# Performance work log

Measured on AMD Instinct MI355X. Metric: run time of the kernel, lower is better.

Reference implementation:

```python
import jax, jax.numpy as jnp
import numpy as np

B, N, D, H = 32, 512, 1024, 16
HD = D // H          # head_dim = 64
SEG = 64             # seg_num (router set size, softmax axis)
FACTOR = N           # einsum forces factor == seq_len


def setup_inputs() -> dict:
    key = jax.random.key(0)
    ks = jax.random.split(key, 12)
    s = 0.02
    return {
        "query": jax.random.normal(ks[0], (B, N, D), jnp.float32),
        "key":   jax.random.normal(ks[1], (B, N, D), jnp.float32),
        "value": jax.random.normal(ks[2], (B, N, D), jnp.float32),
        "router": jax.random.normal(ks[3], (SEG, FACTOR, HD), jnp.float32),
        "Wq": jax.random.normal(ks[4], (D, D), jnp.float32) * s,
        "bq": jnp.zeros((D,), jnp.float32),
        "Wk": jax.random.normal(ks[5], (D, D), jnp.float32) * s,
        "bk": jnp.zeros((D,), jnp.float32),
        "Wv": jax.random.normal(ks[6], (D, D), jnp.float32) * s,
        "bv": jnp.zeros((D,), jnp.float32),
        "Wo": jax.random.normal(ks[7], (D, D), jnp.float32) * s,
        "bo": jnp.zeros((D,), jnp.float32),
    }


def reference(query, key, value, router, Wq, bq, Wk, bk, Wv, bv, Wo, bo):
    b = query.shape[0]
    q = query @ Wq + bq                      # (B, N, D)
    k = key @ Wk + bk                        # computed but unused (faithful to source)
    v = value @ Wv + bv                      # computed but unused (faithful to source)
    # (B, N, H, HD) -> (B, H, N, HD)
    qh = q.reshape(b, -1, H, HD).transpose(0, 2, 1, 3)
    # torch: einsum('bnhd,bfhd->bnhf', q_bHnd, router_bSFd); shared 'h' = seq/factor
    # scores: (B, H, N, SEG); softmax over router/segment axis
    scores = jnp.einsum('bhnd,snd->bhns', qh, router)
    attn = jax.nn.softmax(scores, axis=-1)   # dropout = identity (eval mode)
    # combine: (B, H, N, HD)
    received = jnp.einsum('bhns,snd->bhnd', attn, router)
    received = received.transpose(0, 2, 1, 3).reshape(b, -1, D)
    output = received @ Wo + bo              # (B, N, D)
    return output, attn
```

## Files before the change

### kernel.cpp

```cpp
#include <hip/hip_runtime.h>

#define DEV __device__ __forceinline__

typedef __attribute__((ext_vector_type(8))) short bf16x8;
typedef __attribute__((ext_vector_type(4))) float f32x4;

constexpr int Bc  = 32;
constexpr int Nc  = 512;
constexpr int Dc  = 1024;
constexpr int Hc  = 16;
constexpr int HDc = 64;
constexpr int SEGc= 64;
constexpr int Mrows = Bc * Nc;

DEV unsigned short bf16r(float x) {
  union { float f; unsigned int u; } c; c.f = x;
  unsigned int r = (c.u + 0x7fffu + ((c.u >> 16) & 1u)) >> 16;
  return (unsigned short)r;
}

DEV void async_ld16(const void* g, void* l) {
  __builtin_amdgcn_global_load_lds(
      (const __attribute__((address_space(1))) void*)g,
      (__attribute__((address_space(3))) void*)l,
      16, 0, 0);
}

__global__ __launch_bounds__(256)
void prep(const float* __restrict__ Wq, const float* __restrict__ Wo,
          const float* __restrict__ router,
          unsigned short* __restrict__ wqt, unsigned short* __restrict__ WoT,
          unsigned short* __restrict__ Rg, unsigned short* __restrict__ RTg) {
  const int bid = blockIdx.x;
  if (bid < 2048) {
    __shared__ float tile[32][33];
    const bool isWq = bid < 1024;
    const int b2 = isWq ? bid : bid - 1024;
    const float* src = isWq ? Wq : Wo;
    const int bx = b2 & 31, by = b2 >> 5;
    const int tx = threadIdx.x & 31, ty = threadIdx.x >> 5;
    for (int i = 0; i < 4; ++i) {
      int r = ty + i * 8;
      tile[r][tx] = src[(size_t)(by * 32 + r) * 1024 + bx * 32 + tx];
    }
    __syncthreads();
    if (isWq) {
      if (ty < 4) {
        const int oct = ty;
        const int c = bx * 32 + tx, cbb = c >> 9, cl = c & 511;
        const int cphys = cl ^ (oct << 1);
        unsigned short tmp[8];
#pragma unroll
        for (int e = 0; e < 8; ++e) tmp[e] = bf16r(tile[oct * 8 + e][tx]);
        ushort4 u0, u1;
        u0.x = tmp[0]; u0.y = tmp[1]; u0.z = tmp[2]; u0.w = tmp[3];
        u1.x = tmp[4]; u1.y = tmp[5]; u1.z = tmp[6]; u1.w = tmp[7];
        size_t idx = (size_t)cbb * 524288 + (size_t)by * 16384
                   + (size_t)oct * 4096 + (size_t)cphys * 8;
        *(ushort4*)(wqt + idx)     = u0;
        *(ushort4*)(wqt + idx + 4) = u1;
      }
    } else {
      for (int i = 0; i < 4; ++i) {
        int r = ty + i * 8;
        WoT[(size_t)(bx * 32 + r) * 1024 + by * 32 + tx] = bf16r(tile[tx][r]);
      }
    }
  } else {
    const int nn = bid - 2048;
    const int t  = threadIdx.x;
    const int s  = t >> 2, dq = (t & 3) * 16;
    const float* p = router + ((size_t)s * 512 + nn) * 64 + dq;
    float v[16];
#pragma unroll
    for (int i = 0; i < 16; i += 4) {
      float4 f = *(const float4*)(p + i);
      v[i] = f.x; v[i+1] = f.y; v[i+2] = f.z; v[i+3] = f.w;
    }
    unsigned short bvv[16];
#pragma unroll
    for (int i = 0; i < 16; ++i) bvv[i] = bf16r(v[i]);
    unsigned short* rb = Rg + (size_t)nn * 4096 + s * 64;
#pragma unroll
    for (int o2 = 0; o2 < 2; ++o2) {
      int oct  = (dq >> 3) + o2;
      int phys = oct ^ (s & 7);
      ushort4 a, b2v;
      a.x   = bvv[o2*8+0]; a.y   = bvv[o2*8+1]; a.z   = bvv[o2*8+2]; a.w   = bvv[o2*8+3];
      b2v.x = bvv[o2*8+4]; b2v.y = bvv[o2*8+5]; b2v.z = bvv[o2*8+6]; b2v.w = bvv[o2*8+7];
      *(ushort4*)(rb + phys * 8)     = a;
      *(ushort4*)(rb + phys * 8 + 4) = b2v;
    }
    unsigned short* tb = RTg + (size_t)nn * 4096;
#pragma unroll
    for (int i = 0; i < 16; ++i) {
      int d = dq + i;
      tb[d * 64 + (((s >> 3) ^ (d & 7)) * 8) + (s & 7)] = bvv[i];
    }
  }
}

template <bool OUT_F32>
__global__ __launch_bounds__(256)
void gemm_bt(const unsigned short* __restrict__ A,
             const unsigned short* __restrict__ BT,
             const float* __restrict__ bias,
             void* __restrict__ Cout) {
  constexpr int K = 1024, Nn = 1024, BM = 128, BK = 32;
  __shared__ unsigned short As[BM * BK];
  __shared__ unsigned short Bs[BM * BK];
  const int tid = threadIdx.x, lane = tid & 63, wave = tid >> 6;
  const int tm = blockIdx.x >> 3, tn = blockIdx.x & 7;
  const int wm = (wave >> 1) * 64, wn = (wave & 1) * 64;
  const int la = lane & 15, quad = lane >> 4, lb8 = quad * 8;

  f32x4 acc[4][4] = {};

  const int srow = tid >> 2;
  const int scol = (tid & 3) * 8;
  const unsigned short* Ag = A  + (size_t)(tm * BM + srow) * K + scol;
  const unsigned short* Bg = BT + (size_t)(tn * BM + srow) * K + scol;
  unsigned short* ldsA = As + wave * 512;
  unsigned short* ldsB = Bs + wave * 512;

  for (int k0 = 0; k0 < K; k0 += BK) {
    __syncthreads();
    async_ld16(Ag + k0,          ldsA);
    async_ld16(Ag + 64 * K + k0, ldsA + 2048);
    async_ld16(Bg + k0,          ldsB);
    async_ld16(Bg + 64 * K + k0, ldsB + 2048);
    __syncthreads();

    bf16x8 af[4], bfr[4];
#pragma unroll
    for (int i = 0; i < 4; ++i)
      af[i] = *(const bf16x8*)(As + (wm + i * 16 + la) * BK + lb8);
#pragma unroll
    for (int j = 0; j < 4; ++j)
      bfr[j] = *(const bf16x8*)(Bs + (wn + j * 16 + la) * BK + lb8);
#pragma unroll
    for (int i = 0; i < 4; ++i)
#pragma unroll
      for (int j = 0; j < 4; ++j)
        acc[i][j] = __builtin_amdgcn_mfma_f32_16x16x32_bf16(af[i], bfr[j],
                                                            acc[i][j], 0, 0, 0);
  }

  const int colbase = tn * BM + wn;
  float bv[4];
#pragma unroll
  for (int j = 0; j < 4; ++j) bv[j] = bias[colbase + j * 16 + la];

  float* eps = (wave < 2) ? ((float*)As) + wave * 1024
                          : ((float*)Bs) + (wave - 2) * 1024;
  const int rowbase = tm * BM + wm;

#pragma unroll
  for (int i = 0; i < 4; ++i) {
    __syncthreads();
#pragma unroll
    for (int j = 0; j < 4; ++j)
#pragma unroll
      for (int r = 0; r < 4; ++r)
        eps[(quad * 4 + r) * 64 + j * 16 + la] = acc[i][j][r] + bv[j];
    __syncthreads();
#pragma unroll
    for (int s = 0; s < 4; ++s) {
      int idx = s * 64 + lane;
      int row = idx >> 4, c4 = idx & 15;
      float4 v = *(const float4*)(eps + row * 64 + c4 * 4);
      size_t goff = (size_t)(rowbase + i * 16 + row) * Nn + colbase + c4 * 4;
      if (OUT_F32) {
        *(float4*)((float*)Cout + goff) = v;
      } else {
        ushort4 u;
        u.x = bf16r(v.x); u.y = bf16r(v.y); u.z = bf16r(v.z); u.w = bf16r(v.w);
        *(ushort4*)((unsigned short*)Cout + goff) = u;
      }
    }
  }
}

__global__ __launch_bounds__(512)
void fused_qmid(const float* __restrict__ query,
                const unsigned short* __restrict__ wqt,
                const float* __restrict__ bq,
                const unsigned short* __restrict__ Rg,
                const unsigned short* __restrict__ RTg,
                float* __restrict__ attn_out,
                unsigned short* __restrict__ recv_out) {
  __shared__ __align__(16) unsigned short lds[36864];
  const int tid = threadIdx.x, lane = tid & 63, w = tid >> 6;
  const int la = lane & 15, quad = lane >> 4;
  const int n0 = (blockIdx.x >> 1) * 2, cbh = blockIdx.x & 1;

  f32x4 acc[4][4] = {};

  const int arow = tid >> 3;
  const int ag   = tid & 7;
  const int a_b  = arow & 31, a_nl = arow >> 5;
  const float* aq = query + ((size_t)(a_b * 512 + n0 + a_nl)) * 1024 + ag * 4;
  const int a_oct  = ag >> 1;
  const int a_lidx = a_oct * 512 + (arow ^ (a_oct << 1)) * 8 + (ag & 1) * 4;
  const int bslot  = w * 512 + lane * 8;
  const unsigned short* wqb = wqt + (size_t)cbh * 524288;

  {
    float4 qv = *(const float4*)(aq);
#pragma unroll
    for (int p = 0; p < 4; ++p)
      async_ld16(wqb + p * 4096 + bslot, lds + p * 4096 + w * 512);
    ushort4 u;
    u.x = bf16r(qv.x); u.y = bf16r(qv.y); u.z = bf16r(qv.z); u.w = bf16r(qv.w);
    *(ushort4*)(lds + 32768 + a_lidx) = u;
  }
  __syncthreads();

#pragma unroll 1
  for (int kb = 0; kb < 32; ++kb) {
    const int cur = kb & 1;
    unsigned short* Bc_ = lds + cur * 16384;
    unsigned short* Ac_ = lds + 32768 + cur * 2048;
    unsigned short* Bn_ = lds + (cur ^ 1) * 16384;
    unsigned short* An_ = lds + 32768 + (cur ^ 1) * 2048;

    float4 qv;
    if (kb < 31) {
      qv = *(const float4*)(aq + (kb + 1) * 32);
#pragma unroll
      for (int p = 0; p < 4; ++p)
        async_ld16(wqb + (size_t)(kb + 1) * 16384 + p * 4096 + bslot,
                   Bn_ + p * 4096 + w * 512);
    } else {
#pragma unroll
      for (int q2 = 0; q2 < 4; ++q2) {
        const unsigned short* srcb = (q2 < 2)
            ? (Rg  + (size_t)(n0 + q2)     * 4096)
            : (RTg + (size_t)(n0 + q2 - 2) * 4096);
        async_ld16(srcb + bslot, lds + q2 * 4096 + w * 512);
      }
    }

    bf16x8 af[4], bfr[4];
#pragma unroll
    for (int rt = 0; rt < 4; ++rt)
      af[rt] = *(const bf16x8*)(Ac_ + quad * 512
                                + ((rt * 16 + la) ^ (quad << 1)) * 8);
#pragma unroll
    for (int j = 0; j < 4; ++j)
      bfr[j] = *(const bf16x8*)(Bc_ + quad * 4096
                                + (((w * 4 + j) * 16 + la) ^ (quad << 1)) * 8);
#pragma unroll
    for (int rt = 0; rt < 4; ++rt)
#pragma unroll
      for (int j = 0; j < 4; ++j)
        acc[rt][j] = __builtin_amdgcn_mfma_f32_16x16x32_bf16(af[rt], bfr[j],
                                                             acc[rt][j], 0, 0, 0);
    if (kb < 31) {
      ushort4 u;
      u.x = bf16r(qv.x); u.y = bf16r(qv.y); u.z = bf16r(qv.z); u.w = bf16r(qv.w);
      *(ushort4*)(An_ + a_lidx) = u;
    }
    __syncthreads();
  }

  float bv[4];
#pragma unroll
  for (int j = 0; j < 4; ++j) bv[j] = bq[cbh * 512 + (w * 4 + j) * 16 + la];
#pragma unroll
  for (int rt = 0; rt < 4; ++rt)
#pragma unroll
    for (int j = 0; j < 4; ++j)
#pragma unroll
      for (int r = 0; r < 4; ++r) acc[rt][j][r] += bv[j];

  const int h = cbh * 8 + w;
  unsigned short* QA = lds + 16384 + w * 2304;

#pragma unroll
  for (int nl = 0; nl < 2; ++nl) {
    const int nn = n0 + nl;

#pragma unroll
    for (int rt2 = 0; rt2 < 2; ++rt2)
#pragma unroll
      for (int j4 = 0; j4 < 4; ++j4)
#pragma unroll
        for (int r = 0; r < 4; ++r)
          QA[(rt2 * 16 + quad * 4 + r) * 72 + j4 * 16 + la]
              = bf16r(acc[nl * 2 + rt2][j4][r]);

    bf16x8 qf[2][2], rf[4][2];
#pragma unroll
    for (int bt = 0; bt < 2; ++bt)
#pragma unroll
      for (int kc = 0; kc < 2; ++kc)
        qf[bt][kc] = *(const bf16x8*)(QA + (bt * 16 + la) * 72
                                      + (kc * 4 + quad) * 8);
    const unsigned short* Rn = lds + nl * 4096;
#pragma unroll
    for (int st = 0; st < 4; ++st)
#pragma unroll
      for (int kc = 0; kc < 2; ++kc) {
        int s_ = st * 16 + la;
        rf[st][kc] = *(const bf16x8*)(Rn + s_ * 64
                                      + ((kc * 4 + quad) ^ (s_ & 7)) * 8);
      }

    f32x4 sacc[2][4] = {};
#pragma unroll
    for (int bt = 0; bt < 2; ++bt)
#pragma unroll
      for (int st = 0; st < 4; ++st) {
        sacc[bt][st] = __builtin_amdgcn_mfma_f32_16x16x32_bf16(rf[st][0], qf[bt][0], sacc[bt][st], 0, 0, 0);
        sacc[bt][st] = __builtin_amdgcn_mfma_f32_16x16x32_bf16(rf[st][1], qf[bt][1], sacc[bt][st], 0, 0, 0);
      }

#pragma unroll
    for (int bt = 0; bt < 2; ++bt) {
      float mx = sacc[bt][0][0];
#pragma unroll
      for (int st = 0; st < 4; ++st)
#pragma unroll
        for (int r = 0; r < 4; ++r) mx = fmaxf(mx, sacc[bt][st][r]);
      mx = fmaxf(mx, __shfl_xor(mx, 16));
      mx = fmaxf(mx, __shfl_xor(mx, 32));
      float sum = 0.f;
#pragma unroll
      for (int st = 0; st < 4; ++st)
#pragma unroll
        for (int r = 0; r < 4; ++r) {
          float e = __expf(sacc[bt][st][r] - mx);
          sacc[bt][st][r] = e; sum += e;
        }
      sum += __shfl_xor(sum, 16);
      sum += __shfl_xor(sum, 32);
      float inv = 1.0f / sum;
#pragma unroll
      for (int st = 0; st < 4; ++st) {
        sacc[bt][st][0] *= inv; sacc[bt][st][1] *= inv;
        sacc[bt][st][2] *= inv; sacc[bt][st][3] *= inv;
      }
      const int b_ = bt * 16 + la;
      float* ao = attn_out + ((size_t)(b_ * 16 + h) * 512 + nn) * 64 + quad * 4;
#pragma unroll
      for (int st = 0; st < 4; ++st) {
        *(float4*)(ao + st * 16) = *(float4*)(&sacc[bt][st]);
        ushort4 u;
        u.x = bf16r(sacc[bt][st][0]); u.y = bf16r(sacc[bt][st][1]);
        u.z = bf16r(sacc[bt][st][2]); u.w = bf16r(sacc[bt][st][3]);
        *(ushort4*)(QA + b_ * 72 + st * 16 + quad * 4) = u;
      }
    }

    __asm__ volatile("s_waitcnt lgkmcnt(0)" ::: "memory");
    bf16x8 atf[2][2], rtf2[4][2];
#pragma unroll
    for (int bt = 0; bt < 2; ++bt)
#pragma unroll
      for (int kc = 0; kc < 2; ++kc)
        atf[bt][kc] = *(const bf16x8*)(QA + (bt * 16 + la) * 72
                                       + (kc * 4 + quad) * 8);
    const unsigned short* RTn = lds + 8192 + nl * 4096;
#pragma unroll
    for (int dt = 0; dt < 4; ++dt)
#pragma unroll
      for (int kc = 0; kc < 2; ++kc) {
        int d_ = dt * 16 + la;
        rtf2[dt][kc] = *(const bf16x8*)(RTn + d_ * 64
                                        + ((kc * 4 + quad) ^ (d_ & 7)) * 8);
      }
    f32x4 racc[2][4] = {};
#pragma unroll
    for (int bt = 0; bt < 2; ++bt)
#pragma unroll
      for (int dt = 0; dt < 4; ++dt) {
        racc[bt][dt] = __builtin_amdgcn_mfma_f32_16x16x32_bf16(rtf2[dt][0], atf[bt][0], racc[bt][dt], 0, 0, 0);
        racc[bt][dt] = __builtin_amdgcn_mfma_f32_16x16x32_bf16(rtf2[dt][1], atf[bt][1], racc[bt][dt], 0, 0, 0);
      }

#pragma unroll
    for (int bt = 0; bt < 2; ++bt) {
      const int b_ = bt * 16 + la;
      unsigned short* ro = recv_out + ((size_t)(b_ * 512 + nn)) * 1024
                         + h * 64 + quad * 4;
#pragma unroll
      for (int dt = 0; dt < 4; ++dt) {
        ushort4 u;
        u.x = bf16r(racc[bt][dt][0]); u.y = bf16r(racc[bt][dt][1]);
        u.z = bf16r(racc[bt][dt][2]); u.w = bf16r(racc[bt][dt][3]);
        *(ushort4*)(ro + dt * 16) = u;
      }
    }
  }
}

extern "C" void kernel_launch(void* const* d_in, const int* in_sizes, int n_in,
                              void* d_out, int out_size, void* d_ws, size_t ws_size,
                              hipStream_t stream) {
  const float* query  = (const float*)d_in[0];
  const float* router = (const float*)d_in[3];
  const float* Wq     = (const float*)d_in[4];
  const float* bq     = (const float*)d_in[5];
  const float* Wo     = (const float*)d_in[10];
  const float* bo     = (const float*)d_in[11];

  float* out      = (float*)d_out;
  float* attn_out = out + (size_t)Bc * Nc * Dc;

  char* ws = (char*)d_ws;
  unsigned short* recv_b = (unsigned short*)(ws);
  unsigned short* WqTile = (unsigned short*)(ws + 33554432u);
  unsigned short* WoT    = (unsigned short*)(ws + 35651584u);
  unsigned short* Rg     = (unsigned short*)(ws + 37748736u);
  unsigned short* RTg    = (unsigned short*)(ws + 41943040u);

  prep         <<<2560, 256, 0, stream>>>(Wq, Wo, router, WqTile, WoT, Rg, RTg);
  fused_qmid   <<<512,  512, 0, stream>>>(query, WqTile, bq, Rg, RTg,
                                          attn_out, recv_b);
  gemm_bt<true><<<(Mrows / 128) * 8, 256, 0, stream>>>(recv_b, WoT, bo, out);
}
```

Measured before the change: 378.9 us.

## Pre-convert query to bf16 and pipeline GEMMs with register A-fragments

The prep kernel now also converts the fp32 query to bf16, and Wo is repacked into a swizzled tiled layout. Both GEMM kernels load A fragments straight from global memory into registers and double-buffer only B in per-wave LDS. They wait with s_waitcnt vmcnt instead of block-wide barriers inside the K loop. This is meant to drop the per-iteration __syncthreads and the in-loop fp32-to-bf16 conversion, and to halve query read bandwidth in the main kernel. The cost is an extra 32 MB bf16 write plus re-read of query, and a wider occupancy hint in the launch bounds.

```diff
diff --git a/kernel.cpp b/kernel.cpp
--- a/kernel.cpp
+++ b/kernel.cpp
@@ -28,9 +28,10 @@
 
 __global__ __launch_bounds__(256)
 void prep(const float* __restrict__ Wq, const float* __restrict__ Wo,
-          const float* __restrict__ router,
-          unsigned short* __restrict__ wqt, unsigned short* __restrict__ WoT,
-          unsigned short* __restrict__ Rg, unsigned short* __restrict__ RTg) {
+          const float* __restrict__ router, const float* __restrict__ query,
+          unsigned short* __restrict__ wqt, unsigned short* __restrict__ wot,
+          unsigned short* __restrict__ Rg, unsigned short* __restrict__ RTg,
+          unsigned short* __restrict__ qb) {
   const int bid = blockIdx.x;
   if (bid < 2048) {
     __shared__ float tile[32][33];
@@ -44,29 +45,29 @@
       tile[r][tx] = src[(size_t)(by * 32 + r) * 1024 + bx * 32 + tx];
     }
     __syncthreads();
-    if (isWq) {
-      if (ty < 4) {
-        const int oct = ty;
-        const int c = bx * 32 + tx, cbb = c >> 9, cl = c & 511;
-        const int cphys = cl ^ (oct << 1);
-        unsigned short tmp[8];
-#pragma unroll
-        for (int e = 0; e < 8; ++e) tmp[e] = bf16r(tile[oct * 8 + e][tx]);
-        ushort4 u0, u1;
-        u0.x = tmp[0]; u0.y = tmp[1]; u0.z = tmp[2]; u0.w = tmp[3];
-        u1.x = tmp[4]; u1.y = tmp[5]; u1.z = tmp[6]; u1.w = tmp[7];
-        size_t idx = (size_t)cbb * 524288 + (size_t)by * 16384
-                   + (size_t)oct * 4096 + (size_t)cphys * 8;
-        *(ushort4*)(wqt + idx)     = u0;
-        *(ushort4*)(wqt + idx + 4) = u1;
-      }
-    } else {
-      for (int i = 0; i < 4; ++i) {
-        int r = ty + i * 8;
-        WoT[(size_t)(bx * 32 + r) * 1024 + by * 32 + tx] = bf16r(tile[tx][r]);
-      }
-    }
-  } else {
+    if (ty < 4) {
+      const int oct = ty;
+      const int c = bx * 32 + tx;
+      unsigned short tmp[8];
+#pragma unroll
+      for (int e = 0; e < 8; ++e) tmp[e] = bf16r(tile[oct * 8 + e][tx]);
+      ushort4 u0, u1;
+      u0.x = tmp[0]; u0.y = tmp[1]; u0.z = tmp[2]; u0.w = tmp[3];
+      u1.x = tmp[4]; u1.y = tmp[5]; u1.z = tmp[6]; u1.w = tmp[7];
+      size_t idx;
+      if (isWq) {
+        const int cbb = c >> 9, cl = c & 511;
+        idx = (size_t)cbb * 524288 + (size_t)by * 16384
+            + (size_t)oct * 4096 + (size_t)(cl ^ (oct << 1)) * 8;
+        *(ushort4*)(wqt + idx) = u0; *(ushort4*)(wqt + idx + 4) = u1;
+      } else {
+        const int tn = c >> 7, cl = c & 127;
+        idx = (size_t)tn * 131072 + (size_t)by * 4096
+            + (size_t)oct * 1024 + (size_t)(cl ^ (oct << 1)) * 8;
+        *(ushort4*)(wot + idx) = u0; *(ushort4*)(wot + idx + 4) = u1;
+      }
+    }
+  } else if (bid < 2560) {
     const int nn = bid - 2048;
     const int t  = threadIdx.x;
     const int s  = t >> 2, dq = (t & 3) * 16;
@@ -97,63 +98,91 @@
       int d = dq + i;
       tb[d * 64 + (((s >> 3) ^ (d & 7)) * 8) + (s & 7)] = bvv[i];
     }
-  }
-}
-
-template <bool OUT_F32>
-__global__ __launch_bounds__(256)
+  } else {
+    const size_t base = ((size_t)(bid - 2560) * 256 + threadIdx.x) * 8;
+    float4 a = *(const float4*)(query + base);
+    float4 b = *(const float4*)(query + base + 4);
+    ushort4 u0, u1;
+    u0.x = bf16r(a.x); u0.y = bf16r(a.y); u0.z = bf16r(a.z); u0.w = bf16r(a.w);
+    u1.x = bf16r(b.x); u1.y = bf16r(b.y); u1.z = bf16r(b.z); u1.w = bf16r(b.w);
+    *(ushort4*)(qb + base)     = u0;
+    *(ushort4*)(qb + base + 4) = u1;
+  }
+}
+
+__global__ __launch_bounds__(256, 4)
 void gemm_bt(const unsigned short* __restrict__ A,
-             const unsigned short* __restrict__ BT,
+             const unsigned short* __restrict__ wot,
              const float* __restrict__ bias,
-             void* __restrict__ Cout) {
-  constexpr int K = 1024, Nn = 1024, BM = 128, BK = 32;
-  __shared__ unsigned short As[BM * BK];
-  __shared__ unsigned short Bs[BM * BK];
+             float* __restrict__ Cout) {
+  __shared__ __align__(16) unsigned short lds[16384];
   const int tid = threadIdx.x, lane = tid & 63, wave = tid >> 6;
   const int tm = blockIdx.x >> 3, tn = blockIdx.x & 7;
   const int wm = (wave >> 1) * 64, wn = (wave & 1) * 64;
-  const int la = lane & 15, quad = lane >> 4, lb8 = quad * 8;
+  const int la = lane & 15, quad = lane >> 4;
 
   f32x4 acc[4][4] = {};
 
-  const int srow = tid >> 2;
-  const int scol = (tid & 3) * 8;
-  const unsigned short* Ag = A  + (size_t)(tm * BM + srow) * K + scol;
-  const unsigned short* Bg = BT + (size_t)(tn * BM + srow) * K + scol;
-  unsigned short* ldsA = As + wave * 512;
-  unsigned short* ldsB = Bs + wave * 512;
-
-  for (int k0 = 0; k0 < K; k0 += BK) {
-    __syncthreads();
-    async_ld16(Ag + k0,          ldsA);
-    async_ld16(Ag + 64 * K + k0, ldsA + 2048);
-    async_ld16(Bg + k0,          ldsB);
-    async_ld16(Bg + 64 * K + k0, ldsB + 2048);
-    __syncthreads();
-
-    bf16x8 af[4], bfr[4];
-#pragma unroll
-    for (int i = 0; i < 4; ++i)
-      af[i] = *(const bf16x8*)(As + (wm + i * 16 + la) * BK + lb8);
+  const unsigned short* aA[4];
+#pragma unroll
+  for (int rt = 0; rt < 4; ++rt)
+    aA[rt] = A + (size_t)(tm * 128 + wm + rt * 16 + la) * 1024 + quad * 8;
+  const unsigned short* wob = wot + (size_t)tn * 131072 + wn * 8 + lane * 8;
+  unsigned short* wlds = lds + wave * 2048;
+
+  bf16x8 afA[4], afB[4];
+  {
+#pragma unroll
+    for (int rt = 0; rt < 4; ++rt) afA[rt] = *(const bf16x8*)(aA[rt]);
+#pragma unroll
+    for (int p = 0; p < 4; ++p)
+      async_ld16(wob + p * 1024, wlds + p * 512);
+  }
+  __builtin_amdgcn_sched_barrier(0);
+
+  auto step = [&](int kb, bf16x8* afc, bf16x8* afn,
+                  unsigned short* Bc_, unsigned short* Bn_,
+                  bool last) __attribute__((always_inline)) {
+    if (!last) {
+#pragma unroll
+      for (int rt = 0; rt < 4; ++rt)
+        afn[rt] = *(const bf16x8*)(aA[rt] + (kb + 1) * 32);
+#pragma unroll
+      for (int p = 0; p < 4; ++p)
+        async_ld16(wob + (size_t)(kb + 1) * 4096 + p * 1024, Bn_ + p * 512);
+    }
+    __builtin_amdgcn_sched_barrier(0);
+    if (!last) asm volatile("s_waitcnt vmcnt(8)" ::: "memory");
+    else       asm volatile("s_waitcnt vmcnt(0)" ::: "memory");
+    __builtin_amdgcn_sched_barrier(0);
+    bf16x8 bfr[4];
 #pragma unroll
     for (int j = 0; j < 4; ++j)
-      bfr[j] = *(const bf16x8*)(Bs + (wn + j * 16 + la) * BK + lb8);
-#pragma unroll
-    for (int i = 0; i < 4; ++i)
+      bfr[j] = *(const bf16x8*)(Bc_ + quad * 512
+                                + ((j * 16 + la) ^ (quad << 1)) * 8);
+#pragma unroll
+    for (int rt = 0; rt < 4; ++rt)
 #pragma unroll
       for (int j = 0; j < 4; ++j)
-        acc[i][j] = __builtin_amdgcn_mfma_f32_16x16x32_bf16(af[i], bfr[j],
-                                                            acc[i][j], 0, 0, 0);
-  }
-
-  const int colbase = tn * BM + wn;
+        acc[rt][j] = __builtin_amdgcn_mfma_f32_16x16x32_bf16(afc[rt], bfr[j],
+                                                             acc[rt][j], 0, 0, 0);
+  };
+
+#pragma unroll 1
+  for (int kb = 0; kb < 30; kb += 2) {
+    step(kb,     afA, afB, wlds,        wlds + 8192, false);
+    step(kb + 1, afB, afA, wlds + 8192, wlds,        false);
+  }
+  step(30, afA, afB, wlds,        wlds + 8192, false);
+  step(31, afB, afA, wlds + 8192, wlds,        true);
+
+  const int colbase = tn * 128 + wn;
   float bv[4];
 #pragma unroll
   for (int j = 0; j < 4; ++j) bv[j] = bias[colbase + j * 16 + la];
 
-  float* eps = (wave < 2) ? ((float*)As) + wave * 1024
-                          : ((float*)Bs) + (wave - 2) * 1024;
-  const int rowbase = tm * BM + wm;
+  float* eps = ((float*)lds) + wave * 1024;
+  const int rowbase = tm * 128 + wm;
 
 #pragma unroll
   for (int i = 0; i < 4; ++i) {
@@ -169,100 +198,82 @@
       int idx = s * 64 + lane;
       int row = idx >> 4, c4 = idx & 15;
       float4 v = *(const float4*)(eps + row * 64 + c4 * 4);
-      size_t goff = (size_t)(rowbase + i * 16 + row) * Nn + colbase + c4 * 4;
-      if (OUT_F32) {
-        *(float4*)((float*)Cout + goff) = v;
-      } else {
-        ushort4 u;
-        u.x = bf16r(v.x); u.y = bf16r(v.y); u.z = bf16r(v.z); u.w = bf16r(v.w);
-        *(ushort4*)((unsigned short*)Cout + goff) = u;
-      }
-    }
-  }
-}
-
-__global__ __launch_bounds__(512)
-void fused_qmid(const float* __restrict__ query,
+      *(float4*)(Cout + (size_t)(rowbase + i * 16 + row) * 1024
+                 + colbase + c4 * 4) = v;
+    }
+  }
+}
+
+__global__ __launch_bounds__(512, 4)
+void fused_qmid(const unsigned short* __restrict__ qb,
                 const unsigned short* __restrict__ wqt,
                 const float* __restrict__ bq,
                 const unsigned short* __restrict__ Rg,
                 const unsigned short* __restrict__ RTg,
                 float* __restrict__ attn_out,
                 unsigned short* __restrict__ recv_out) {
-  __shared__ __align__(16) unsigned short lds[36864];
+  __shared__ __align__(16) unsigned short lds[34816];
   const int tid = threadIdx.x, lane = tid & 63, w = tid >> 6;
   const int la = lane & 15, quad = lane >> 4;
   const int n0 = (blockIdx.x >> 1) * 2, cbh = blockIdx.x & 1;
 
   f32x4 acc[4][4] = {};
 
-  const int arow = tid >> 3;
-  const int ag   = tid & 7;
-  const int a_b  = arow & 31, a_nl = arow >> 5;
-  const float* aq = query + ((size_t)(a_b * 512 + n0 + a_nl)) * 1024 + ag * 4;
-  const int a_oct  = ag >> 1;
-  const int a_lidx = a_oct * 512 + (arow ^ (a_oct << 1)) * 8 + (ag & 1) * 4;
-  const int bslot  = w * 512 + lane * 8;
-  const unsigned short* wqb = wqt + (size_t)cbh * 524288;
-
+  const unsigned short* aA[4];
+#pragma unroll
+  for (int rt = 0; rt < 4; ++rt) {
+    int rho = rt * 16 + la;
+    aA[rt] = qb + ((size_t)((rho & 31) * 512 + n0 + (rho >> 5))) * 1024
+           + quad * 8;
+  }
+  const unsigned short* wqb = wqt + (size_t)cbh * 524288 + w * 512 + lane * 8;
+  unsigned short* wlds = lds + w * 512;
+
+  bf16x8 afA[4], afB[4];
   {
-    float4 qv = *(const float4*)(aq);
+#pragma unroll
+    for (int rt = 0; rt < 4; ++rt) afA[rt] = *(const bf16x8*)(aA[rt]);
 #pragma unroll
     for (int p = 0; p < 4; ++p)
-      async_ld16(wqb + p * 4096 + bslot, lds + p * 4096 + w * 512);
-    ushort4 u;
-    u.x = bf16r(qv.x); u.y = bf16r(qv.y); u.z = bf16r(qv.z); u.w = bf16r(qv.w);
-    *(ushort4*)(lds + 32768 + a_lidx) = u;
-  }
-  __syncthreads();
-
-#pragma unroll 1
-  for (int kb = 0; kb < 32; ++kb) {
-    const int cur = kb & 1;
-    unsigned short* Bc_ = lds + cur * 16384;
-    unsigned short* Ac_ = lds + 32768 + cur * 2048;
-    unsigned short* Bn_ = lds + (cur ^ 1) * 16384;
-    unsigned short* An_ = lds + 32768 + (cur ^ 1) * 2048;
-
-    float4 qv;
-    if (kb < 31) {
-      qv = *(const float4*)(aq + (kb + 1) * 32);
+      async_ld16(wqb + p * 4096, wlds + p * 4096);
+  }
+  __builtin_amdgcn_sched_barrier(0);
+
+  auto step = [&](int kb, bf16x8* afc, bf16x8* afn,
+                  unsigned short* Bc_, unsigned short* Bn_,
+                  bool last) __attribute__((always_inline)) {
+    if (!last) {
+#pragma unroll
+      for (int rt = 0; rt < 4; ++rt)
+        afn[rt] = *(const bf16x8*)(aA[rt] + (kb + 1) * 32);
 #pragma unroll
       for (int p = 0; p < 4; ++p)
-        async_ld16(wqb + (size_t)(kb + 1) * 16384 + p * 4096 + bslot,
-                   Bn_ + p * 4096 + w * 512);
-    } else {
-#pragma unroll
-      for (int q2 = 0; q2 < 4; ++q2) {
-        const unsigned short* srcb = (q2 < 2)
-            ? (Rg  + (size_t)(n0 + q2)     * 4096)
-            : (RTg + (size_t)(n0 + q2 - 2) * 4096);
-        async_ld16(srcb + bslot, lds + q2 * 4096 + w * 512);
-      }
-    }
-
-    bf16x8 af[4], bfr[4];
-#pragma unroll
-    for (int rt = 0; rt < 4; ++rt)
-      af[rt] = *(const bf16x8*)(Ac_ + quad * 512
-                                + ((rt * 16 + la) ^ (quad << 1)) * 8);
+        async_ld16(wqb + (size_t)(kb + 1) * 16384 + p * 4096, Bn_ + p * 4096);
+    }
+    __builtin_amdgcn_sched_barrier(0);
+    if (!last) asm volatile("s_waitcnt vmcnt(8)" ::: "memory");
+    else       asm volatile("s_waitcnt vmcnt(0)" ::: "memory");
+    __builtin_amdgcn_sched_barrier(0);
+    bf16x8 bfr[4];
 #pragma unroll
     for (int j = 0; j < 4; ++j)
       bfr[j] = *(const bf16x8*)(Bc_ + quad * 4096
-                                + (((w * 4 + j) * 16 + la) ^ (quad << 1)) * 8);
+                                + ((j * 16 + la) ^ (quad << 1)) * 8);
 #pragma unroll
     for (int rt = 0; rt < 4; ++rt)
 #pragma unroll
       for (int j = 0; j < 4; ++j)
-        acc[rt][j] = __builtin_amdgcn_mfma_f32_16x16x32_bf16(af[rt], bfr[j],
+        acc[rt][j] = __builtin_amdgcn_mfma_f32_16x16x32_bf16(afc[rt], bfr[j],
                                                              acc[rt][j], 0, 0, 0);
-    if (kb < 31) {
-      ushort4 u;
-      u.x = bf16r(qv.x); u.y = bf16r(qv.y); u.z = bf16r(qv.z); u.w = bf16r(qv.w);
-      *(ushort4*)(An_ + a_lidx) = u;
-    }
-    __syncthreads();
-  }
+  };
+
+#pragma unroll 1
+  for (int kb = 0; kb < 30; kb += 2) {
+    step(kb,     afA, afB, wlds,         wlds + 16384, false);
+    step(kb + 1, afB, afA, wlds + 16384, wlds,         false);
+  }
+  step(30, afA, afB, wlds,         wlds + 16384, false);
+  step(31, afB, afA, wlds + 16384, wlds,         true);
 
   float bv[4];
 #pragma unroll
@@ -273,6 +284,19 @@
     for (int j = 0; j < 4; ++j)
 #pragma unroll
       for (int r = 0; r < 4; ++r) acc[rt][j][r] += bv[j];
+
+  __syncthreads();
+  {
+    const int bslot = w * 512 + lane * 8;
+#pragma unroll
+    for (int q2 = 0; q2 < 4; ++q2) {
+      const unsigned short* srcb = (q2 < 2)
+          ? (Rg  + (size_t)(n0 + q2)     * 4096)
+          : (RTg + (size_t)(n0 + q2 - 2) * 4096);
+      async_ld16(srcb + bslot, lds + q2 * 4096 + w * 512);
+    }
+  }
+  __syncthreads();
 
   const int h = cbh * 8 + w;
   unsigned short* QA = lds + 16384 + w * 2304;
@@ -409,14 +433,16 @@
   float* attn_out = out + (size_t)Bc * Nc * Dc;
 
   char* ws = (char*)d_ws;
-  unsigned short* recv_b = (unsigned short*)(ws);
-  unsigned short* WqTile = (unsigned short*)(ws + 33554432u);
-  unsigned short* WoT    = (unsigned short*)(ws + 35651584u);
-  unsigned short* Rg     = (unsigned short*)(ws + 37748736u);
-  unsigned short* RTg    = (unsigned short*)(ws + 41943040u);
-
-  prep         <<<2560, 256, 0, stream>>>(Wq, Wo, router, WqTile, WoT, Rg, RTg);
-  fused_qmid   <<<512,  512, 0, stream>>>(query, WqTile, bq, Rg, RTg,
-                                          attn_out, recv_b);
-  gemm_bt<true><<<(Mrows / 128) * 8, 256, 0, stream>>>(recv_b, WoT, bo, out);
-}
+  unsigned short* recv_b  = (unsigned short*)(ws);
+  unsigned short* query_b = (unsigned short*)(ws + 33554432u);
+  unsigned short* WqTile  = (unsigned short*)(ws + 67108864u);
+  unsigned short* WoTile  = (unsigned short*)(ws + 69206016u);
+  unsigned short* Rg      = (unsigned short*)(ws + 71303168u);
+  unsigned short* RTg     = (unsigned short*)(ws + 75497472u);
+
+  prep      <<<10752, 256, 0, stream>>>(Wq, Wo, router, query,
+                                        WqTile, WoTile, Rg, RTg, query_b);
+  fused_qmid<<<512,   512, 0, stream>>>(query_b, WqTile, bq, Rg, RTg,
+                                        attn_out, recv_b);
+  gemm_bt   <<<(Mrows / 128) * 8, 256, 0, stream>>>(recv_b, WoTile, bo, out);
+}
```

After: 557.7 us. 1.47x slower.
